# Kernel tuning notes

Hardware: AMD Instinct MI355X
Metric: run time of the kernel (lower is better)

Reference implementation:

```python
import jax, jax.numpy as jnp
import numpy as np

B, N, S, HEADS, D = 8, 512, 64, 16, 256

def setup_inputs() -> dict:
    key = jax.random.key(0)
    ks = jax.random.split(key, 5)
    spatial_pos = jax.random.randint(ks[0], (B, N, S), 0, N)
    H = jax.random.normal(ks[1], (B, N, D), dtype=jnp.float32)
    A = jax.random.uniform(ks[2], (B, N, N), dtype=jnp.float32)
    sigma = jnp.ones((1,), dtype=jnp.float32)
    spatial_emb = jax.random.normal(ks[3], (N, HEADS), dtype=jnp.float32)
    vt_weight = jax.random.normal(ks[4], (1, HEADS), dtype=jnp.float32)
    return {"spatial_pos": spatial_pos, "H": H, "A": A, "sigma": sigma,
            "spatial_emb": spatial_emb, "vt_weight": vt_weight}

def reference(spatial_pos, H, A, sigma, spatial_emb, vt_weight):
    b, n, s = spatial_pos.shape
    heads = spatial_emb.shape[1]
    # padding_idx=0: row 0 of the embedding table is zero
    emb = spatial_emb.at[0].set(0.0)
    spb = emb[spatial_pos]                       # [B, N, S, heads]
    # torch .view reinterprets contiguous memory: reshape, NOT transpose
    spb = spb.reshape(b, heads, n, s)            # [B, heads, N, S]
    spatial_bias = jnp.einsum('bhns,bhms->bhnm', spb, spb)  # [B,heads,N,N]
    # degree-normalized (left) adjacency aggregation
    deg = jnp.sum(A, axis=-1, keepdims=True)     # [B, N, 1]
    nor_A = (deg ** -0.5) * A
    M = jnp.matmul(nor_A, H)                     # [B, N, D]
    # pairwise squared euclidean distance via expansion (same math,
    # avoids materializing [B,N,N,D])
    h2 = jnp.sum(H * H, axis=-1)                 # [B, N]
    m2 = jnp.sum(M * M, axis=-1)                 # [B, N]
    cross = jnp.einsum('bnd,bmd->bnm', H, M)     # [B, N, N]
    d2 = h2[:, :, None] + m2[:, None, :] - 2.0 * cross
    gaussian = jnp.exp(-d2 / (2.0 * sigma[0] ** 2))  # [B, N, N]
    # virtual-token bias (vt_weight) only touches padded row/col 0,
    # which is sliced off before return -> no effect on output.
    return spatial_bias + gaussian[:, None, :, :]  # [B, heads, N, N]
```

## Files before the change

### kernel.cpp

```cpp
#include <hip/hip_runtime.h>
#include <hip/hip_bf16.h>

#define NB 8
#define NN 512
#define NS 64
#define NH 16
#define ND 256

typedef __attribute__((ext_vector_type(8))) short bf16x8;
typedef __attribute__((ext_vector_type(4))) short bf16x4;
typedef __attribute__((ext_vector_type(4))) float f32x4;

__device__ inline float wred(float v) {
#pragma unroll
  for (int m = 32; m; m >>= 1) v += __shfl_xor(v, m, 64);
  return v;
}
__device__ inline float wred16(float v) {
#pragma unroll
  for (int m = 1; m < 16; m <<= 1) v += __shfl_xor(v, m, 64);
  return v;
}
__device__ inline ushort f2bf(float x) {
  __hip_bfloat16 h = __float2bfloat16(x);
  return *(ushort*)&h;
}

__global__ __launch_bounds__(256) void k_prep(const int* __restrict__ pos,
                                              const float* __restrict__ emb,
                                              const float* __restrict__ H,
                                              const float* __restrict__ A,
                                              __hip_bfloat16* __restrict__ spb,
                                              __hip_bfloat16* __restrict__ Ab,
                                              __hip_bfloat16* __restrict__ Hb,
                                              __hip_bfloat16* __restrict__ HT,
                                              float* __restrict__ rdeg,
                                              float* __restrict__ h2) {
  __shared__ ushort T[64][68];
  int blk = blockIdx.x, tid = threadIdx.x;
  int wave = tid >> 6, lane = tid & 63;

  if (blk < 1024) {
    int t = blk * 256 + tid;
    int idx = pos[t];
    __hip_bfloat16* dst = spb + (size_t)t * NH;
    union { bf16x8 v; ushort h[8]; } u0, u1;
    if (idx == 0) {
#pragma unroll
      for (int i = 0; i < 8; ++i) { u0.h[i] = 0; u1.h[i] = 0; }
    } else {
      const float* er = emb + idx * NH;
      float4 e0 = *(const float4*)(er);
      float4 e1 = *(const float4*)(er + 4);
      float4 e2 = *(const float4*)(er + 8);
      float4 e3 = *(const float4*)(er + 12);
      u0.h[0] = f2bf(e0.x); u0.h[1] = f2bf(e0.y); u0.h[2] = f2bf(e0.z); u0.h[3] = f2bf(e0.w);
      u0.h[4] = f2bf(e1.x); u0.h[5] = f2bf(e1.y); u0.h[6] = f2bf(e1.z); u0.h[7] = f2bf(e1.w);
      u1.h[0] = f2bf(e2.x); u1.h[1] = f2bf(e2.y); u1.h[2] = f2bf(e2.z); u1.h[3] = f2bf(e2.w);
      u1.h[4] = f2bf(e3.x); u1.h[5] = f2bf(e3.y); u1.h[6] = f2bf(e3.z); u1.h[7] = f2bf(e3.w);
    }
    *(bf16x8*)(void*)dst = u0.v;
    *(bf16x8*)(void*)(dst + 8) = u1.v;
  } else if (blk < 2048) {
    int row = (blk - 1024) * 4 + wave;
    const float* ar = A + (size_t)row * NN;
    float4 v0 = *(const float4*)(ar + lane * 8);
    float4 v1 = *(const float4*)(ar + lane * 8 + 4);
    float s = v0.x + v0.y + v0.z + v0.w + v1.x + v1.y + v1.z + v1.w;
    union { bf16x8 v; ushort h[8]; } u;
    u.h[0] = f2bf(v0.x); u.h[1] = f2bf(v0.y); u.h[2] = f2bf(v0.z); u.h[3] = f2bf(v0.w);
    u.h[4] = f2bf(v1.x); u.h[5] = f2bf(v1.y); u.h[6] = f2bf(v1.z); u.h[7] = f2bf(v1.w);
    *(bf16x8*)(void*)(Ab + (size_t)row * NN + lane * 8) = u.v;
    s = wred(s);
    if (lane == 0) rdeg[row] = rsqrtf(s);
  } else if (blk < 3072) {
    int row = (blk - 2048) * 4 + wave;
    const float* hr = H + (size_t)row * ND;
    float4 v = *(const float4*)(hr + lane * 4);
    float ss = v.x * v.x + v.y * v.y + v.z * v.z + v.w * v.w;
    union { bf16x4 v4; ushort h[4]; } u;
    u.h[0] = f2bf(v.x); u.h[1] = f2bf(v.y); u.h[2] = f2bf(v.z); u.h[3] = f2bf(v.w);
    *(bf16x4*)(void*)(Hb + (size_t)row * ND + lane * 4) = u.v4;
    ss = wred(ss);
    if (lane == 0) h2[row] = ss;
  } else {
    int bi = blk - 3072;
    int b = bi >> 5, r = bi & 31;
    int d0 = (r >> 3) * 64, n0 = (r & 7) * 64;
    int n = tid >> 2, c = (tid & 3) * 16;
    const float* src = H + ((size_t)b * NN + n0 + n) * ND + d0 + c;
#pragma unroll
    for (int q = 0; q < 4; ++q) {
      float4 f = *(const float4*)(src + q * 4);
      T[n][c + q * 4 + 0] = f2bf(f.x);
      T[n][c + q * 4 + 1] = f2bf(f.y);
      T[n][c + q * 4 + 2] = f2bf(f.z);
      T[n][c + q * 4 + 3] = f2bf(f.w);
    }
    __syncthreads();
    int d = tid >> 2, nc = (tid & 3) * 16;
    union { bf16x8 v; ushort h[8]; } o0, o1;
#pragma unroll
    for (int i = 0; i < 8; ++i) { o0.h[i] = T[nc + i][d]; o1.h[i] = T[nc + 8 + i][d]; }
    __hip_bfloat16* dst = HT + ((size_t)b * ND + d0 + d) * NN + n0 + nc;
    *(bf16x8*)(void*)dst = o0.v;
    *(bf16x8*)(void*)(dst + 8) = o1.v;
  }
}

__global__ __launch_bounds__(256) void k_gemmM(const __hip_bfloat16* __restrict__ Ab,
                                               const __hip_bfloat16* __restrict__ HT,
                                               const float* __restrict__ rdeg,
                                               __hip_bfloat16* __restrict__ Mb,
                                               float* __restrict__ m2p) {
  int wave = threadIdx.x >> 6, lane = threadIdx.x & 63;
  int b = blockIdx.x & 7, t = blockIdx.x >> 3;
  int tile = t * 4 + wave;
  int rt = tile >> 3, ct = tile & 7;
  int r0 = rt * 16, c0 = ct * 32;
  int rl = lane & 15, g4 = lane >> 4;
  const __hip_bfloat16* X = Ab + (size_t)b * NN * NN;
  const __hip_bfloat16* Y = HT + (size_t)b * ND * NN;
  f32x4 acc[2];
#pragma unroll
  for (int j = 0; j < 2; ++j) { acc[j][0] = 0.f; acc[j][1] = 0.f; acc[j][2] = 0.f; acc[j][3] = 0.f; }
#pragma unroll
  for (int kk = 0; kk < NN / 32; ++kk) {
    int kb = kk * 32 + g4 * 8;
    bf16x8 a = *(const bf16x8*)(const void*)(X + (size_t)(r0 + rl) * NN + kb);
#pragma unroll
    for (int j = 0; j < 2; ++j) {
      bf16x8 bv = *(const bf16x8*)(const void*)(Y + (size_t)(c0 + j * 16 + rl) * NN + kb);
      acc[j] = __builtin_amdgcn_mfma_f32_16x16x32_bf16(a, bv, acc[j], 0, 0, 0);
    }
  }
#pragma unroll
  for (int r = 0; r < 4; ++r) {
    int row = r0 + g4 * 4 + r;
    float rd = rdeg[b * NN + row];
    float ss = 0.f;
#pragma unroll
    for (int j = 0; j < 2; ++j) {
      float m = rd * acc[j][r];
      int col = c0 + j * 16 + rl;
      Mb[((size_t)b * NN + row) * ND + col] = __float2bfloat16(m);
      ss += m * m;
    }
    ss = wred16(ss);
    if (rl == 0) m2p[(size_t)ct * (NB * NN) + b * NN + row] = ss;
  }
}

__global__ __launch_bounds__(256) void k_out(const __hip_bfloat16* __restrict__ Hb,
                                             const __hip_bfloat16* __restrict__ Mb,
                                             const __hip_bfloat16* __restrict__ spb,
                                             const float* __restrict__ h2,
                                             const float* __restrict__ m2p,
                                             const float* __restrict__ sigma,
                                             float* __restrict__ out) {
  __shared__ __align__(16) float Gt[64][68];
  __shared__ __align__(16) float Ot[4][16][72];
  __shared__ float h2s[64], m2s[64];
  int b = blockIdx.x & 7;
  int t2 = blockIdx.x >> 3;
  int ct = t2 & 7, rt = t2 >> 3;
  int r0 = rt * 64, c0 = ct * 64;
  int tid = threadIdx.x;
  int wave = tid >> 6, lane = tid & 63;
  int rl = lane & 15, g4 = lane >> 4;

  if (tid < 64) {
    h2s[tid] = h2[b * NN + r0 + tid];
  } else if (tid < 128) {
    int c = tid - 64;
    float s = 0.f;
#pragma unroll
    for (int p = 0; p < 8; ++p) s += m2p[(size_t)p * (NB * NN) + b * NN + c0 + c];
    m2s[c] = s;
  }
  __syncthreads();

  {
    const __hip_bfloat16* X = Hb + (size_t)b * NN * ND;
    const __hip_bfloat16* Y = Mb + (size_t)b * NN * ND;
    int rw = wave * 16;
    f32x4 acc[4];
#pragma unroll
    for (int j = 0; j < 4; ++j) { acc[j][0] = 0.f; acc[j][1] = 0.f; acc[j][2] = 0.f; acc[j][3] = 0.f; }
#pragma unroll
    for (int kk = 0; kk < ND / 32; ++kk) {
      int kb = kk * 32 + g4 * 8;
      bf16x8 a = *(const bf16x8*)(const void*)(X + (size_t)(r0 + rw + rl) * ND + kb);
#pragma unroll
      for (int j = 0; j < 4; ++j) {
        bf16x8 bv = *(const bf16x8*)(const void*)(Y + (size_t)(c0 + j * 16 + rl) * ND + kb);
        acc[j] = __builtin_amdgcn_mfma_f32_16x16x32_bf16(a, bv, acc[j], 0, 0, 0);
      }
    }
    float sg = sigma[0];
    float inv = 0.5f / (sg * sg);
#pragma unroll
    for (int j = 0; j < 4; ++j)
#pragma unroll
      for (int r = 0; r < 4; ++r) {
        int rowl = rw + g4 * 4 + r;
        int col = j * 16 + rl;
        float d2 = h2s[rowl] + m2s[col] - 2.0f * acc[j][r];
        Gt[rowl][col] = __expf(-d2 * inv);
      }
  }
  __syncthreads();

  f32x4 greg[4][4];
#pragma unroll
  for (int i = 0; i < 4; ++i)
#pragma unroll
    for (int j = 0; j < 4; ++j)
      greg[i][j] = *(const f32x4*)&Gt[i * 16 + rl][j * 16 + g4 * 4];

  float (*Ow)[72] = Ot[wave];
#pragma unroll 1
  for (int hh = 0; hh < 4; ++hh) {
    int h = wave * 4 + hh;
    const __hip_bfloat16* Xs = spb + ((size_t)b * NH + h) * NN * NS;
    f32x4 acc[4][4];
#pragma unroll
    for (int i = 0; i < 4; ++i)
#pragma unroll
      for (int j = 0; j < 4; ++j) { acc[i][j][0] = 0.f; acc[i][j][1] = 0.f; acc[i][j][2] = 0.f; acc[i][j][3] = 0.f; }
#pragma unroll
    for (int kk = 0; kk < NS / 32; ++kk) {
      int kb = kk * 32 + g4 * 8;
      bf16x8 a[4], bv[4];
#pragma unroll
      for (int i = 0; i < 4; ++i)
        a[i] = *(const bf16x8*)(const void*)(Xs + (size_t)(r0 + i * 16 + rl) * NS + kb);
#pragma unroll
      for (int j = 0; j < 4; ++j)
        bv[j] = *(const bf16x8*)(const void*)(Xs + (size_t)(c0 + j * 16 + rl) * NS + kb);
#pragma unroll
      for (int i = 0; i < 4; ++i)
#pragma unroll
        for (int j = 0; j < 4; ++j)
          acc[i][j] = __builtin_amdgcn_mfma_f32_16x16x32_bf16(bv[j], a[i], acc[i][j], 0, 0, 0);
    }
    float* ob = out + ((size_t)b * NH + h) * NN * NN;
#pragma unroll
    for (int i = 0; i < 4; ++i) {
#pragma unroll
      for (int j = 0; j < 4; ++j) {
        f32x4 w = acc[i][j] + greg[i][j];
        *(f32x4*)&Ow[rl][j * 16 + g4 * 4] = w;
      }
      asm volatile("s_waitcnt lgkmcnt(0)" ::: "memory");
#pragma unroll
      for (int it = 0; it < 4; ++it) {
        int row = it * 4 + g4;
        int col = rl * 4;
        float4 o = *(const float4*)&Ow[row][col];
        *(float4*)&ob[(size_t)(r0 + i * 16 + row) * NN + c0 + col] = o;
      }
      asm volatile("" ::: "memory");
    }
  }
}

extern "C" void kernel_launch(void* const* d_in, const int* in_sizes, int n_in,
                              void* d_out, int out_size, void* d_ws, size_t ws_size,
                              hipStream_t stream) {
  const int* pos = (const int*)d_in[0];
  const float* H = (const float*)d_in[1];
  const float* A = (const float*)d_in[2];
  const float* sigma = (const float*)d_in[3];
  const float* emb = (const float*)d_in[4];
  float* out = (float*)d_out;

  char* ws = (char*)d_ws;
  size_t off = 0;
  auto alloc = [&](size_t bytes) -> void* {
    void* p = ws + off;
    off = (off + bytes + 255) & ~(size_t)255;
    return p;
  };
  __hip_bfloat16* spb = (__hip_bfloat16*)alloc((size_t)NB * NH * NN * NS * 2);
  __hip_bfloat16* Ab  = (__hip_bfloat16*)alloc((size_t)NB * NN * NN * 2);
  __hip_bfloat16* Hb  = (__hip_bfloat16*)alloc((size_t)NB * NN * ND * 2);
  __hip_bfloat16* HT  = (__hip_bfloat16*)alloc((size_t)NB * ND * NN * 2);
  __hip_bfloat16* Mb  = (__hip_bfloat16*)alloc((size_t)NB * NN * ND * 2);
  float* m2p  = (float*)alloc((size_t)8 * NB * NN * 4);
  float* rdeg = (float*)alloc((size_t)NB * NN * 4);
  float* h2   = (float*)alloc((size_t)NB * NN * 4);

  k_prep<<<3328, 256, 0, stream>>>(pos, emb, H, A, spb, Ab, Hb, HT, rdeg, h2);
  k_gemmM<<<512, 256, 0, stream>>>(Ab, HT, rdeg, Mb, m2p);
  k_out<<<512, 256, 0, stream>>>(Hb, Mb, spb, h2, m2p, sigma, out);
}
```

Baseline: 63.11 us.

## Split spatial-bias work by row strips per wave across all heads

Each wave used to compute the full 64x64 tile for 4 of the 16 heads. Now each wave owns a 16-row strip of the tile and loops over all 16 heads. This cuts per-wave accumulators and gaussian registers from 16 fragments to 4, which can raise occupancy and shrink register pressure. In exchange, every wave reloads the B-operand column fragments for every head, and there are four times as many loop iterations with less MFMA work each.

```diff
diff --git a/kernel.cpp b/kernel.cpp
--- a/kernel.cpp
+++ b/kernel.cpp
@@ -180,10 +180,10 @@
   }
   __syncthreads();
 
+  int rw = wave * 16;
   {
     const __hip_bfloat16* X = Hb + (size_t)b * NN * ND;
     const __hip_bfloat16* Y = Mb + (size_t)b * NN * ND;
-    int rw = wave * 16;
     f32x4 acc[4];
 #pragma unroll
     for (int j = 0; j < 4; ++j) { acc[j][0] = 0.f; acc[j][1] = 0.f; acc[j][2] = 0.f; acc[j][3] = 0.f; }
@@ -211,57 +211,43 @@
   }
   __syncthreads();
 
-  f32x4 greg[4][4];
-#pragma unroll
-  for (int i = 0; i < 4; ++i)
-#pragma unroll
-    for (int j = 0; j < 4; ++j)
-      greg[i][j] = *(const f32x4*)&Gt[i * 16 + rl][j * 16 + g4 * 4];
+  f32x4 greg[4];
+#pragma unroll
+  for (int j = 0; j < 4; ++j)
+    greg[j] = *(const f32x4*)&Gt[rw + rl][j * 16 + g4 * 4];
 
   float (*Ow)[72] = Ot[wave];
-#pragma unroll 1
-  for (int hh = 0; hh < 4; ++hh) {
-    int h = wave * 4 + hh;
+#pragma unroll 2
+  for (int h = 0; h < NH; ++h) {
     const __hip_bfloat16* Xs = spb + ((size_t)b * NH + h) * NN * NS;
-    f32x4 acc[4][4];
-#pragma unroll
-    for (int i = 0; i < 4; ++i)
-#pragma unroll
-      for (int j = 0; j < 4; ++j) { acc[i][j][0] = 0.f; acc[i][j][1] = 0.f; acc[i][j][2] = 0.f; acc[i][j][3] = 0.f; }
+    f32x4 acc[4];
+#pragma unroll
+    for (int j = 0; j < 4; ++j) { acc[j][0] = 0.f; acc[j][1] = 0.f; acc[j][2] = 0.f; acc[j][3] = 0.f; }
 #pragma unroll
     for (int kk = 0; kk < NS / 32; ++kk) {
       int kb = kk * 32 + g4 * 8;
-      bf16x8 a[4], bv[4];
-#pragma unroll
-      for (int i = 0; i < 4; ++i)
-        a[i] = *(const bf16x8*)(const void*)(Xs + (size_t)(r0 + i * 16 + rl) * NS + kb);
-#pragma unroll
-      for (int j = 0; j < 4; ++j)
-        bv[j] = *(const bf16x8*)(const void*)(Xs + (size_t)(c0 + j * 16 + rl) * NS + kb);
-#pragma unroll
-      for (int i = 0; i < 4; ++i)
-#pragma unroll
-        for (int j = 0; j < 4; ++j)
-          acc[i][j] = __builtin_amdgcn_mfma_f32_16x16x32_bf16(bv[j], a[i], acc[i][j], 0, 0, 0);
+      bf16x8 a = *(const bf16x8*)(const void*)(Xs + (size_t)(r0 + rw + rl) * NS + kb);
+#pragma unroll
+      for (int j = 0; j < 4; ++j) {
+        bf16x8 bv = *(const bf16x8*)(const void*)(Xs + (size_t)(c0 + j * 16 + rl) * NS + kb);
+        acc[j] = __builtin_amdgcn_mfma_f32_16x16x32_bf16(bv, a, acc[j], 0, 0, 0);
+      }
     }
     float* ob = out + ((size_t)b * NH + h) * NN * NN;
 #pragma unroll
-    for (int i = 0; i < 4; ++i) {
-#pragma unroll
-      for (int j = 0; j < 4; ++j) {
-        f32x4 w = acc[i][j] + greg[i][j];
-        *(f32x4*)&Ow[rl][j * 16 + g4 * 4] = w;
-      }
-      asm volatile("s_waitcnt lgkmcnt(0)" ::: "memory");
-#pragma unroll
-      for (int it = 0; it < 4; ++it) {
-        int row = it * 4 + g4;
-        int col = rl * 4;
-        float4 o = *(const float4*)&Ow[row][col];
-        *(float4*)&ob[(size_t)(r0 + i * 16 + row) * NN + c0 + col] = o;
-      }
-      asm volatile("" ::: "memory");
-    }
+    for (int j = 0; j < 4; ++j) {
+      f32x4 w = acc[j] + greg[j];
+      *(f32x4*)&Ow[rl][j * 16 + g4 * 4] = w;
+    }
+    asm volatile("s_waitcnt lgkmcnt(0)" ::: "memory");
+#pragma unroll
+    for (int it = 0; it < 4; ++it) {
+      int row = it * 4 + g4;
+      int col = rl * 4;
+      float4 o = *(const float4*)&Ow[row][col];
+      *(float4*)&ob[(size_t)(r0 + rw + row) * NN + c0 + col] = o;
+    }
+    asm volatile("" ::: "memory");
   }
 }
 
```

Result: slower. 80.36 us (+27.3%).
